# Performance work log

Hardware: AMD Instinct MI355X
Metric: run time of the kernel (lower is better)

The kernel has to match this reference:

```python
import jax, jax.numpy as jnp
import numpy as np

# Scene / model dims (match init_kwargs)
H, W, T = 128, 128, 8
N = 1024  # number of 3D (x,y,t) Gaussians, layer 0

CHOL_BOUND_3D = jnp.array([0.5, 0.0, 0.5, 0.5, 0.0, 0.5], dtype=jnp.float32)


def setup_inputs() -> dict:
    key = jax.random.key(0)
    k1, k2, k3 = jax.random.split(key, 3)
    xyz = jax.random.normal(k1, (N, 3), dtype=jnp.float32)          # raw (pre-tanh) positions
    cholesky = jax.random.uniform(k2, (N, 6), dtype=jnp.float32)    # raw cholesky params
    cholesky = cholesky.at[:, 5].add(float(T))                      # _init_layer0: data[:,5] += T
    features = jax.random.uniform(k3, (N, 3), dtype=jnp.float32)    # rgb features
    opacity = jnp.ones((N, 1), dtype=jnp.float32)                   # layer-0 opacity buffer (ones)
    background = jnp.ones((3,), dtype=jnp.float32)                  # unused by the sum-rasterizer
    return {"xyz": xyz, "cholesky": cholesky, "features": features,
            "opacity": opacity, "background": background}


def _render(xyz, cholesky, features, opacity):
    # --- project_gaussians_video ---
    # positions: tanh -> ndc (-1,1) -> pixel/frame coords (ndc2pix: 0.5*((v+1)*S - 1))
    sizes = jnp.array([W, H, T], dtype=jnp.float32)
    means = 0.5 * ((jnp.tanh(xyz) + 1.0) * sizes - 1.0)             # (N,3) in (x,y,t)
    c = cholesky + CHOL_BOUND_3D                                     # get_cholesky_elements
    # lower-triangular L, column-major packing: [L00,L10,L20,L11,L21,L22]
    L = jnp.zeros((N, 3, 3), dtype=c.dtype)
    L = L.at[:, 0, 0].set(c[:, 0]).at[:, 1, 0].set(c[:, 1]).at[:, 2, 0].set(c[:, 2])
    L = L.at[:, 1, 1].set(c[:, 3]).at[:, 2, 1].set(c[:, 4]).at[:, 2, 2].set(c[:, 5])
    cov = jnp.einsum('nij,nkj->nik', L, L)                           # Sigma = L L^T
    conic = jnp.linalg.inv(cov)                                      # (N,3,3), symmetric

    # --- rasterize_gaussians_sum_video (dense reference, no tile culling) ---
    # sigma(p) = 0.5 p^T Q p - p^T Q m + 0.5 m^T Q m, expressed as a [P,10] x [10,N] matmul
    qm = jnp.einsum('nij,nj->ni', conic, means)                      # (N,3)
    const = 0.5 * jnp.einsum('ni,ni->n', means, qm)                  # (N,)
    G = jnp.stack([0.5 * conic[:, 0, 0], 0.5 * conic[:, 1, 1], 0.5 * conic[:, 2, 2],
                   conic[:, 0, 1], conic[:, 0, 2], conic[:, 1, 2],
                   -qm[:, 0], -qm[:, 1], -qm[:, 2], const], axis=1)  # (N,10)

    ts = jnp.arange(T, dtype=jnp.float32)
    ys = jnp.arange(H, dtype=jnp.float32)
    xs = jnp.arange(W, dtype=jnp.float32)
    pt, py, px = jnp.meshgrid(ts, ys, xs, indexing='ij')             # (T,H,W) — t-major pixel order
    px, py, pt = px.ravel(), py.ravel(), pt.ravel()                  # (P,), P = T*H*W
    F = jnp.stack([px * px, py * py, pt * pt, px * py, px * pt, py * pt,
                   px, py, pt, jnp.ones_like(px)], axis=1)           # (P,10)

    sigma = F @ G.T                                                  # (P,N) — memory-bound hot loop
    wgt = jnp.exp(-sigma) * opacity[:, 0][None, :]                   # alpha per pixel/gaussian
    img = wgt @ features                                             # (P,3) alpha-weighted sum blend
    img = jnp.clip(img, 0.0, 1.0)
    # view(-1,T,H,W,3).permute(0,4,2,3,1) -> (1,3,H,W,T)
    return jnp.transpose(img.reshape(1, T, H, W, 3), (0, 4, 2, 3, 1))


def reference(xyz, cholesky, features, opacity, background):
    return _render(xyz, cholesky, features, opacity)
```

## Files before the change

### kernel.cpp

```cpp
#include <hip/hip_runtime.h>
#include <math.h>

#define HH 128
#define WW 128
#define TT 8
#define NG 1024
#define PP (HH * WW * TT)

__device__ __forceinline__ float fast_tanh(float x) {
    float e = __builtin_amdgcn_exp2f(x * 2.885390081777926814f);
    return 1.f - 2.f * __builtin_amdgcn_rcpf(e + 1.f);
}

__global__ __launch_bounds__(256) void gv_fused(
    const float* __restrict__ xyz,
    const float* __restrict__ chol,
    const float* __restrict__ feat,
    const float* __restrict__ opac,
    float* __restrict__ out)
{
    __shared__ __align__(16) float recs[NG * 8];
    __shared__ int sidx[NG];
    __shared__ int cnt_lds[4];

    const int tid = threadIdx.x;
    const int lane = tid & 63;
    const int wv = tid >> 6;
    const int r0 = blockIdx.x * 2;
    const float y0f = (float)(r0 & 127);
    const float tf  = (float)(r0 >> 7);
    const float kneg = -1.44269504088896340736f;

    int S_run = 0;
    for (int it = 0; it < NG / 256; ++it) {
        const int n = it * 256 + tid;
        float vy = xyz[n * 3 + 1];
        float c1 = chol[n * 6 + 1];
        float c3 = chol[n * 6 + 3] + 0.5f;
        float my = fmaf(fast_tanh(vy), 64.f, 63.5f);
        float syy = fmaf(c1, c1, c3 * c3);
        float d0 = my - y0f;
        float d1 = d0 - 1.f;
        float dmin = fminf(fabsf(d0), fabsf(d1));
        bool keep = dmin * dmin < 32.f * syy;

        unsigned long long mask = __ballot(keep);
        if (lane == 0) cnt_lds[wv] = (int)__popcll(mask);
        __syncthreads();
        int base = S_run;
        for (int w = 0; w < wv; ++w) base += cnt_lds[w];
        int tot = cnt_lds[0] + cnt_lds[1] + cnt_lds[2] + cnt_lds[3];
        if (keep) {
            int pos = __builtin_amdgcn_mbcnt_hi(
                          (unsigned)(mask >> 32),
                          __builtin_amdgcn_mbcnt_lo((unsigned)mask, 0));
            sidx[base + pos] = n;
        }
        S_run += tot;
        __syncthreads();
    }
    const int S = S_run;

    for (int j = tid; j < S; j += 256) {
        const int n = sidx[j];
        float vx = xyz[n * 3 + 0], vy = xyz[n * 3 + 1], vt = xyz[n * 3 + 2];
        float mx = 0.5f * ((fast_tanh(vx) + 1.f) * (float)WW - 1.f);
        float my = 0.5f * ((fast_tanh(vy) + 1.f) * (float)HH - 1.f);
        float mt = 0.5f * ((fast_tanh(vt) + 1.f) * (float)TT - 1.f);

        float c0 = chol[n * 6 + 0] + 0.5f;
        float c1 = chol[n * 6 + 1];
        float c2 = chol[n * 6 + 2] + 0.5f;
        float c3 = chol[n * 6 + 3] + 0.5f;
        float c4 = chol[n * 6 + 4];
        float c5 = chol[n * 6 + 5] + 0.5f;

        float a  = c0 * c0;
        float b  = c0 * c1;
        float cc = c0 * c2;
        float d  = c1 * c1 + c3 * c3;
        float e  = c1 * c2 + c3 * c4;
        float f  = c2 * c2 + c4 * c4 + c5 * c5;

        float A00 = d * f - e * e;
        float A01 = cc * e - b * f;
        float A02 = b * e - cc * d;
        float A11 = a * f - cc * cc;
        float A12 = b * cc - a * e;
        float A22 = a * d - b * b;
        float det = a * A00 + b * A01 + cc * A02;
        float rdet = 1.f / det;
        float Q00 = A00 * rdet, Q01 = A01 * rdet, Q02 = A02 * rdet;
        float Q11 = A11 * rdet, Q12 = A12 * rdet, Q22 = A22 * rdet;

        float qmx = Q00 * mx + Q01 * my + Q02 * mt;
        float qmy = Q01 * mx + Q11 * my + Q12 * mt;
        float qmt = Q02 * mx + Q12 * my + Q22 * mt;
        float cst = 0.5f * (mx * qmx + my * qmy + mt * qmt);

        float G0 = 0.5f * Q00, G1 = 0.5f * Q11, G2 = 0.5f * Q22;
        float G3 = Q01, G4 = Q02, G5 = Q12;
        float G6 = -qmx, G7 = -qmy, G8 = -qmt, G9 = cst;

        float u  = fmaf(G4, tf, G6);
        float v  = fmaf(G5, tf, G7);
        float w0 = fmaf(fmaf(G2, tf, G8), tf, G9);
        float B0 = fmaf(G3, y0f, u);
        float C0 = fmaf(fmaf(G1, y0f, v), y0f, w0);
        float y1f = y0f + 1.f;
        float B1 = fmaf(G3, y1f, u);
        float C1 = fmaf(fmaf(G1, y1f, v), y1f, w0);

        float op = opac[n];
        float4* l4 = (float4*)recs;
        l4[j * 2 + 0] = (float4){kneg * G0, op * feat[n * 3 + 0],
                                 op * feat[n * 3 + 1], op * feat[n * 3 + 2]};
        l4[j * 2 + 1] = (float4){kneg * B0, kneg * C0, kneg * B1, kneg * C1};
    }
    __syncthreads();

    const int rowi = wv >> 1;
    const int x = (wv & 1) * 64 + lane;
    const float xf = (float)x;
    float a0 = 0.f, a1 = 0.f, a2 = 0.f;
    const float4* lds4 = (const float4*)recs;

#pragma unroll 4
    for (int m = 0; m < S; ++m) {
        float4 af = lds4[m * 2];
        float2 bc = *(const float2*)&recs[m * 8 + 4 + 2 * rowi];
        float s = fmaf(fmaf(af.x, xf, bc.x), xf, bc.y);
        float w = __builtin_amdgcn_exp2f(s);
        a0 = fmaf(w, af.y, a0);
        a1 = fmaf(w, af.z, a1);
        a2 = fmaf(w, af.w, a2);
    }

    a0 = fminf(fmaxf(a0, 0.f), 1.f);
    a1 = fminf(fmaxf(a1, 0.f), 1.f);
    a2 = fminf(fmaxf(a2, 0.f), 1.f);

    const int r = r0 + rowi;
    const int y = r & 127, t = r >> 7;
    const int base_o = (y * WW + x) * TT + t;
    out[base_o] = a0;
    out[base_o + PP] = a1;
    out[base_o + 2 * PP] = a2;
}

extern "C" void kernel_launch(void* const* d_in, const int* in_sizes, int n_in,
                              void* d_out, int out_size, void* d_ws, size_t ws_size,
                              hipStream_t stream) {
    const float* xyz  = (const float*)d_in[0];
    const float* chol = (const float*)d_in[1];
    const float* feat = (const float*)d_in[2];
    const float* opac = (const float*)d_in[3];
    float* out = (float*)d_out;

    const int blocks = (TT * HH) / 2;
    gv_fused<<<blocks, 256, 0, stream>>>(xyz, chol, feat, opac, out);
}
```

Before: 14.36 us.

## Split fused kernel into prep pass and main raster pass using workspace

Adds a prep kernel that culls Gaussians per row-pair once, shared across all time frames, and computes each Gaussian's conic and color record once into a workspace buffer. The main kernel then reads the precomputed list and records instead of redoing culling and matrix inversion in each of the 512 blocks. This removes repeated per-block setup work but adds a second launch and global-memory round trips. The original fused kernel remains as a fallback when the workspace is too small. The prep kernel uses tanhf instead of the fast approximation.

```diff
diff --git a/kernel.cpp b/kernel.cpp
--- a/kernel.cpp
+++ b/kernel.cpp
@@ -6,10 +6,181 @@
 #define TT 8
 #define NG 1024
 #define PP (HH * WW * TT)
+#define YP 64
+
+#define REC_OFF    0
+#define SLIST_OFF  (NG * 16)
+#define SCOUNT_OFF (SLIST_OFF + YP * NG)
+#define WS_FLOATS  (SCOUNT_OFF + YP)
 
 __device__ __forceinline__ float fast_tanh(float x) {
     float e = __builtin_amdgcn_exp2f(x * 2.885390081777926814f);
     return 1.f - 2.f * __builtin_amdgcn_rcpf(e + 1.f);
+}
+
+__global__ __launch_bounds__(256) void gv_prep(
+    const float* __restrict__ xyz,
+    const float* __restrict__ chol,
+    const float* __restrict__ feat,
+    const float* __restrict__ opac,
+    float* __restrict__ ws)
+{
+    const int bid = blockIdx.x;
+    const int tid = threadIdx.x;
+
+    if (bid < YP) {
+        __shared__ int cnt_lds[4];
+        int* slist = (int*)(ws + SLIST_OFF) + bid * NG;
+        int* scount = (int*)(ws + SCOUNT_OFF);
+        const int lane = tid & 63;
+        const int wv = tid >> 6;
+        const float y0f = (float)(2 * bid);
+
+        int S_run = 0;
+        for (int it = 0; it < NG / 256; ++it) {
+            const int n = it * 256 + tid;
+            float vy = xyz[n * 3 + 1];
+            float c1 = chol[n * 6 + 1];
+            float c3 = chol[n * 6 + 3] + 0.5f;
+            float my = fmaf(tanhf(vy), 64.f, 63.5f);
+            float syy = fmaf(c1, c1, c3 * c3);
+            float d0 = my - y0f;
+            float d1 = d0 - 1.f;
+            float dmin = fminf(fabsf(d0), fabsf(d1));
+            bool keep = dmin * dmin < 32.f * syy;
+
+            unsigned long long mask = __ballot(keep);
+            if (lane == 0) cnt_lds[wv] = (int)__popcll(mask);
+            __syncthreads();
+            int base = S_run;
+            for (int w = 0; w < wv; ++w) base += cnt_lds[w];
+            int tot = cnt_lds[0] + cnt_lds[1] + cnt_lds[2] + cnt_lds[3];
+            if (keep) {
+                int pos = __builtin_amdgcn_mbcnt_hi(
+                              (unsigned)(mask >> 32),
+                              __builtin_amdgcn_mbcnt_lo((unsigned)mask, 0));
+                slist[base + pos] = n;
+            }
+            S_run += tot;
+            __syncthreads();
+        }
+        if (tid == 0) scount[bid] = S_run;
+    } else {
+        const int n = (bid - YP) * 128 + tid;
+        if (tid >= 128) return;
+
+        float vx = xyz[n * 3 + 0], vy = xyz[n * 3 + 1], vt = xyz[n * 3 + 2];
+        float mx = 0.5f * ((tanhf(vx) + 1.f) * (float)WW - 1.f);
+        float my = 0.5f * ((tanhf(vy) + 1.f) * (float)HH - 1.f);
+        float mt = 0.5f * ((tanhf(vt) + 1.f) * (float)TT - 1.f);
+
+        float c0 = chol[n * 6 + 0] + 0.5f;
+        float c1 = chol[n * 6 + 1];
+        float c2 = chol[n * 6 + 2] + 0.5f;
+        float c3 = chol[n * 6 + 3] + 0.5f;
+        float c4 = chol[n * 6 + 4];
+        float c5 = chol[n * 6 + 5] + 0.5f;
+
+        float a  = c0 * c0;
+        float b  = c0 * c1;
+        float cc = c0 * c2;
+        float d  = c1 * c1 + c3 * c3;
+        float e  = c1 * c2 + c3 * c4;
+        float f  = c2 * c2 + c4 * c4 + c5 * c5;
+
+        float A00 = d * f - e * e;
+        float A01 = cc * e - b * f;
+        float A02 = b * e - cc * d;
+        float A11 = a * f - cc * cc;
+        float A12 = b * cc - a * e;
+        float A22 = a * d - b * b;
+        float det = a * A00 + b * A01 + cc * A02;
+        float rdet = 1.f / det;
+        float Q00 = A00 * rdet, Q01 = A01 * rdet, Q02 = A02 * rdet;
+        float Q11 = A11 * rdet, Q12 = A12 * rdet, Q22 = A22 * rdet;
+
+        float qmx = Q00 * mx + Q01 * my + Q02 * mt;
+        float qmy = Q01 * mx + Q11 * my + Q12 * mt;
+        float qmt = Q02 * mx + Q12 * my + Q22 * mt;
+        float cst = 0.5f * (mx * qmx + my * qmy + mt * qmt);
+
+        float op = opac[n];
+        float4* r4 = (float4*)(ws + REC_OFF);
+        r4[n * 4 + 0] = (float4){0.5f * Q00, 0.5f * Q11, 0.5f * Q22, Q01};
+        r4[n * 4 + 1] = (float4){Q02, Q12, -qmx, -qmy};
+        r4[n * 4 + 2] = (float4){-qmt, cst, 0.f, 0.f};
+        r4[n * 4 + 3] = (float4){op * feat[n * 3 + 0], op * feat[n * 3 + 1],
+                                 op * feat[n * 3 + 2], 0.f};
+    }
+}
+
+__global__ __launch_bounds__(256) void gv_main(
+    const float* __restrict__ ws,
+    float* __restrict__ out)
+{
+    __shared__ __align__(16) float recs[NG * 8];
+
+    const int tid = threadIdx.x;
+    const int lane = tid & 63;
+    const int wv = tid >> 6;
+    const int yp = blockIdx.x & 63;
+    const int t  = blockIdx.x >> 6;
+    const float y0f = (float)(2 * yp);
+    const float tf  = (float)t;
+    const float kneg = -1.44269504088896340736f;
+
+    const int* slist = (const int*)(ws + SLIST_OFF) + yp * NG;
+    const int S = ((const int*)(ws + SCOUNT_OFF))[yp];
+    const float4* g4 = (const float4*)(ws + REC_OFF);
+
+    for (int j = tid; j < S; j += 256) {
+        const int n = slist[j];
+        float4 ra = g4[n * 4 + 0];
+        float4 rb = g4[n * 4 + 1];
+        float4 rc = g4[n * 4 + 2];
+        float4 rd = g4[n * 4 + 3];
+
+        float u  = fmaf(rb.x, tf, rb.z);
+        float v  = fmaf(rb.y, tf, rb.w);
+        float w0 = fmaf(fmaf(ra.z, tf, rc.x), tf, rc.y);
+        float B0 = fmaf(ra.w, y0f, u);
+        float C0 = fmaf(fmaf(ra.y, y0f, v), y0f, w0);
+        float y1f = y0f + 1.f;
+        float B1 = fmaf(ra.w, y1f, u);
+        float C1 = fmaf(fmaf(ra.y, y1f, v), y1f, w0);
+
+        float4* l4 = (float4*)recs;
+        l4[j * 2 + 0] = (float4){kneg * ra.x, rd.x, rd.y, rd.z};
+        l4[j * 2 + 1] = (float4){kneg * B0, kneg * C0, kneg * B1, kneg * C1};
+    }
+    __syncthreads();
+
+    const int rowi = wv >> 1;
+    const int x = (wv & 1) * 64 + lane;
+    const float xf = (float)x;
+    float a0 = 0.f, a1 = 0.f, a2 = 0.f;
+    const float4* lds4 = (const float4*)recs;
+
+#pragma unroll 4
+    for (int m = 0; m < S; ++m) {
+        float4 af = lds4[m * 2];
+        float2 bc = *(const float2*)&recs[m * 8 + 4 + 2 * rowi];
+        float s = fmaf(fmaf(af.x, xf, bc.x), xf, bc.y);
+        float w = __builtin_amdgcn_exp2f(s);
+        a0 = fmaf(w, af.y, a0);
+        a1 = fmaf(w, af.z, a1);
+        a2 = fmaf(w, af.w, a2);
+    }
+
+    a0 = fminf(fmaxf(a0, 0.f), 1.f);
+    a1 = fminf(fmaxf(a1, 0.f), 1.f);
+    a2 = fminf(fmaxf(a2, 0.f), 1.f);
+
+    const int y = 2 * yp + rowi;
+    const int base_o = (y * WW + x) * TT + t;
+    out[base_o] = a0;
+    out[base_o + PP] = a1;
+    out[base_o + 2 * PP] = a2;
 }
 
 __global__ __launch_bounds__(256) void gv_fused(
@@ -67,37 +238,26 @@
         float mx = 0.5f * ((fast_tanh(vx) + 1.f) * (float)WW - 1.f);
         float my = 0.5f * ((fast_tanh(vy) + 1.f) * (float)HH - 1.f);
         float mt = 0.5f * ((fast_tanh(vt) + 1.f) * (float)TT - 1.f);
-
         float c0 = chol[n * 6 + 0] + 0.5f;
         float c1 = chol[n * 6 + 1];
         float c2 = chol[n * 6 + 2] + 0.5f;
         float c3 = chol[n * 6 + 3] + 0.5f;
         float c4 = chol[n * 6 + 4];
         float c5 = chol[n * 6 + 5] + 0.5f;
-
-        float a  = c0 * c0;
-        float b  = c0 * c1;
-        float cc = c0 * c2;
+        float a  = c0 * c0, b = c0 * c1, cc = c0 * c2;
         float d  = c1 * c1 + c3 * c3;
         float e  = c1 * c2 + c3 * c4;
         float f  = c2 * c2 + c4 * c4 + c5 * c5;
-
-        float A00 = d * f - e * e;
-        float A01 = cc * e - b * f;
-        float A02 = b * e - cc * d;
-        float A11 = a * f - cc * cc;
-        float A12 = b * cc - a * e;
-        float A22 = a * d - b * b;
+        float A00 = d * f - e * e, A01 = cc * e - b * f, A02 = b * e - cc * d;
+        float A11 = a * f - cc * cc, A12 = b * cc - a * e, A22 = a * d - b * b;
         float det = a * A00 + b * A01 + cc * A02;
         float rdet = 1.f / det;
         float Q00 = A00 * rdet, Q01 = A01 * rdet, Q02 = A02 * rdet;
         float Q11 = A11 * rdet, Q12 = A12 * rdet, Q22 = A22 * rdet;
-
         float qmx = Q00 * mx + Q01 * my + Q02 * mt;
         float qmy = Q01 * mx + Q11 * my + Q12 * mt;
         float qmt = Q02 * mx + Q12 * my + Q22 * mt;
         float cst = 0.5f * (mx * qmx + my * qmy + mt * qmt);
-
         float G0 = 0.5f * Q00, G1 = 0.5f * Q11, G2 = 0.5f * Q22;
         float G3 = Q01, G4 = Q02, G5 = Q12;
         float G6 = -qmx, G7 = -qmy, G8 = -qmt, G9 = cst;
@@ -156,7 +316,12 @@
     const float* feat = (const float*)d_in[2];
     const float* opac = (const float*)d_in[3];
     float* out = (float*)d_out;
-
-    const int blocks = (TT * HH) / 2;
-    gv_fused<<<blocks, 256, 0, stream>>>(xyz, chol, feat, opac, out);
-}
+    float* ws  = (float*)d_ws;
+
+    if (ws_size >= (size_t)WS_FLOATS * sizeof(float)) {
+        gv_prep<<<YP + NG / 128, 256, 0, stream>>>(xyz, chol, feat, opac, ws);
+        gv_main<<<YP * TT, 256, 0, stream>>>(ws, out);
+    } else {
+        gv_fused<<<(TT * HH) / 2, 256, 0, stream>>>(xyz, chol, feat, opac, out);
+    }
+}
```

Result: slower. 17.63 us (+22.7%).

## Split Gaussian list across eight wave groups with LDS partial-sum reduction

Applied to the files above, without the earlier changes.

Each block grows from 256 to 1024 threads. The 1024 Gaussians are split into 8 slices of 128, and each pair of waves culls and preprocesses its own slice without the serial prefix-scan loop and its repeated barriers. Each wave now covers two pixels per lane (x and x+64) and accumulates over only its slice. Partial sums are then reduced through LDS by the first group. This shortens the per-thread serial loop over Gaussians and the culling serialization, at the cost of a larger block, more LDS use, an extra reduction pass and possible load imbalance between slices.

```diff
diff --git a/kernel.cpp b/kernel.cpp
--- a/kernel.cpp
+++ b/kernel.cpp
@@ -6,34 +6,38 @@
 #define TT 8
 #define NG 1024
 #define PP (HH * WW * TT)
+#define NS 8
+#define GS 128
 
 __device__ __forceinline__ float fast_tanh(float x) {
     float e = __builtin_amdgcn_exp2f(x * 2.885390081777926814f);
     return 1.f - 2.f * __builtin_amdgcn_rcpf(e + 1.f);
 }
 
-__global__ __launch_bounds__(256) void gv_fused(
+__global__ __launch_bounds__(1024, 8) void gv_fused(
     const float* __restrict__ xyz,
     const float* __restrict__ chol,
     const float* __restrict__ feat,
     const float* __restrict__ opac,
     float* __restrict__ out)
 {
-    __shared__ __align__(16) float recs[NG * 8];
-    __shared__ int sidx[NG];
-    __shared__ int cnt_lds[4];
+    __shared__ __align__(16) float recs[NS][GS * 8];
+    __shared__ int sidx[NS][GS];
+    __shared__ int cnt_lds[16];
+    __shared__ __align__(16) float4 pbuf[7][2][WW];
 
     const int tid = threadIdx.x;
     const int lane = tid & 63;
     const int wv = tid >> 6;
+    const int s = wv >> 1;
+    const int sub = wv & 1;
     const int r0 = blockIdx.x * 2;
     const float y0f = (float)(r0 & 127);
     const float tf  = (float)(r0 >> 7);
     const float kneg = -1.44269504088896340736f;
 
-    int S_run = 0;
-    for (int it = 0; it < NG / 256; ++it) {
-        const int n = it * 256 + tid;
+    {
+        const int n = s * GS + sub * 64 + lane;
         float vy = xyz[n * 3 + 1];
         float c1 = chol[n * 6 + 1];
         float c3 = chol[n * 6 + 3] + 0.5f;
@@ -45,107 +49,137 @@
         bool keep = dmin * dmin < 32.f * syy;
 
         unsigned long long mask = __ballot(keep);
-        if (lane == 0) cnt_lds[wv] = (int)__popcll(mask);
-        __syncthreads();
-        int base = S_run;
-        for (int w = 0; w < wv; ++w) base += cnt_lds[w];
-        int tot = cnt_lds[0] + cnt_lds[1] + cnt_lds[2] + cnt_lds[3];
         if (keep) {
             int pos = __builtin_amdgcn_mbcnt_hi(
                           (unsigned)(mask >> 32),
                           __builtin_amdgcn_mbcnt_lo((unsigned)mask, 0));
-            sidx[base + pos] = n;
+            sidx[s][sub * 64 + pos] = n;
         }
-        S_run += tot;
-        __syncthreads();
-    }
-    const int S = S_run;
-
-    for (int j = tid; j < S; j += 256) {
-        const int n = sidx[j];
-        float vx = xyz[n * 3 + 0], vy = xyz[n * 3 + 1], vt = xyz[n * 3 + 2];
-        float mx = 0.5f * ((fast_tanh(vx) + 1.f) * (float)WW - 1.f);
-        float my = 0.5f * ((fast_tanh(vy) + 1.f) * (float)HH - 1.f);
-        float mt = 0.5f * ((fast_tanh(vt) + 1.f) * (float)TT - 1.f);
-
-        float c0 = chol[n * 6 + 0] + 0.5f;
-        float c1 = chol[n * 6 + 1];
-        float c2 = chol[n * 6 + 2] + 0.5f;
-        float c3 = chol[n * 6 + 3] + 0.5f;
-        float c4 = chol[n * 6 + 4];
-        float c5 = chol[n * 6 + 5] + 0.5f;
-
-        float a  = c0 * c0;
-        float b  = c0 * c1;
-        float cc = c0 * c2;
-        float d  = c1 * c1 + c3 * c3;
-        float e  = c1 * c2 + c3 * c4;
-        float f  = c2 * c2 + c4 * c4 + c5 * c5;
-
-        float A00 = d * f - e * e;
-        float A01 = cc * e - b * f;
-        float A02 = b * e - cc * d;
-        float A11 = a * f - cc * cc;
-        float A12 = b * cc - a * e;
-        float A22 = a * d - b * b;
-        float det = a * A00 + b * A01 + cc * A02;
-        float rdet = 1.f / det;
-        float Q00 = A00 * rdet, Q01 = A01 * rdet, Q02 = A02 * rdet;
-        float Q11 = A11 * rdet, Q12 = A12 * rdet, Q22 = A22 * rdet;
-
-        float qmx = Q00 * mx + Q01 * my + Q02 * mt;
-        float qmy = Q01 * mx + Q11 * my + Q12 * mt;
-        float qmt = Q02 * mx + Q12 * my + Q22 * mt;
-        float cst = 0.5f * (mx * qmx + my * qmy + mt * qmt);
-
-        float G0 = 0.5f * Q00, G1 = 0.5f * Q11, G2 = 0.5f * Q22;
-        float G3 = Q01, G4 = Q02, G5 = Q12;
-        float G6 = -qmx, G7 = -qmy, G8 = -qmt, G9 = cst;
-
-        float u  = fmaf(G4, tf, G6);
-        float v  = fmaf(G5, tf, G7);
-        float w0 = fmaf(fmaf(G2, tf, G8), tf, G9);
-        float B0 = fmaf(G3, y0f, u);
-        float C0 = fmaf(fmaf(G1, y0f, v), y0f, w0);
-        float y1f = y0f + 1.f;
-        float B1 = fmaf(G3, y1f, u);
-        float C1 = fmaf(fmaf(G1, y1f, v), y1f, w0);
-
-        float op = opac[n];
-        float4* l4 = (float4*)recs;
-        l4[j * 2 + 0] = (float4){kneg * G0, op * feat[n * 3 + 0],
-                                 op * feat[n * 3 + 1], op * feat[n * 3 + 2]};
-        l4[j * 2 + 1] = (float4){kneg * B0, kneg * C0, kneg * B1, kneg * C1};
+        if (lane == 0) cnt_lds[wv] = (int)__popcll(mask);
     }
     __syncthreads();
 
-    const int rowi = wv >> 1;
-    const int x = (wv & 1) * 64 + lane;
-    const float xf = (float)x;
+    {
+        const int sb = tid >> 7;
+        const int tq = tid & 127;
+        const int cA = cnt_lds[2 * sb];
+        const int Sb = cA + cnt_lds[2 * sb + 1];
+        if (tq < Sb) {
+            const int n = (tq < cA) ? sidx[sb][tq] : sidx[sb][64 + tq - cA];
+
+            float vx = xyz[n * 3 + 0], vy = xyz[n * 3 + 1], vt = xyz[n * 3 + 2];
+            float mx = 0.5f * ((fast_tanh(vx) + 1.f) * (float)WW - 1.f);
+            float my = 0.5f * ((fast_tanh(vy) + 1.f) * (float)HH - 1.f);
+            float mt = 0.5f * ((fast_tanh(vt) + 1.f) * (float)TT - 1.f);
+
+            float c0 = chol[n * 6 + 0] + 0.5f;
+            float c1 = chol[n * 6 + 1];
+            float c2 = chol[n * 6 + 2] + 0.5f;
+            float c3 = chol[n * 6 + 3] + 0.5f;
+            float c4 = chol[n * 6 + 4];
+            float c5 = chol[n * 6 + 5] + 0.5f;
+
+            float a  = c0 * c0;
+            float b  = c0 * c1;
+            float cc = c0 * c2;
+            float d  = c1 * c1 + c3 * c3;
+            float e  = c1 * c2 + c3 * c4;
+            float f  = c2 * c2 + c4 * c4 + c5 * c5;
+
+            float A00 = d * f - e * e;
+            float A01 = cc * e - b * f;
+            float A02 = b * e - cc * d;
+            float A11 = a * f - cc * cc;
+            float A12 = b * cc - a * e;
+            float A22 = a * d - b * b;
+            float det = a * A00 + b * A01 + cc * A02;
+            float rdet = 1.f / det;
+            float Q00 = A00 * rdet, Q01 = A01 * rdet, Q02 = A02 * rdet;
+            float Q11 = A11 * rdet, Q12 = A12 * rdet, Q22 = A22 * rdet;
+
+            float qmx = Q00 * mx + Q01 * my + Q02 * mt;
+            float qmy = Q01 * mx + Q11 * my + Q12 * mt;
+            float qmt = Q02 * mx + Q12 * my + Q22 * mt;
+            float cst = 0.5f * (mx * qmx + my * qmy + mt * qmt);
+
+            float G0 = 0.5f * Q00, G1 = 0.5f * Q11, G2 = 0.5f * Q22;
+            float G3 = Q01, G4 = Q02, G5 = Q12;
+            float G6 = -qmx, G7 = -qmy, G8 = -qmt, G9 = cst;
+
+            float u  = fmaf(G4, tf, G6);
+            float v  = fmaf(G5, tf, G7);
+            float w0 = fmaf(fmaf(G2, tf, G8), tf, G9);
+            float B0 = fmaf(G3, y0f, u);
+            float C0 = fmaf(fmaf(G1, y0f, v), y0f, w0);
+            float y1f = y0f + 1.f;
+            float B1 = fmaf(G3, y1f, u);
+            float C1 = fmaf(fmaf(G1, y1f, v), y1f, w0);
+
+            float op = opac[n];
+            float4* l4 = (float4*)recs[sb];
+            l4[tq * 2 + 0] = (float4){kneg * G0, op * feat[n * 3 + 0],
+                                      op * feat[n * 3 + 1], op * feat[n * 3 + 2]};
+            l4[tq * 2 + 1] = (float4){kneg * B0, kneg * C0, kneg * B1, kneg * C1};
+        }
+    }
+    __syncthreads();
+
+    const int S = cnt_lds[2 * s] + cnt_lds[2 * s + 1];
+    const float x1 = (float)lane;
+    const float x2 = x1 + 64.f;
     float a0 = 0.f, a1 = 0.f, a2 = 0.f;
-    const float4* lds4 = (const float4*)recs;
+    float b0 = 0.f, b1 = 0.f, b2 = 0.f;
+    const float4* lds4 = (const float4*)recs[s];
+    const float* recf = recs[s];
 
 #pragma unroll 4
     for (int m = 0; m < S; ++m) {
         float4 af = lds4[m * 2];
-        float2 bc = *(const float2*)&recs[m * 8 + 4 + 2 * rowi];
-        float s = fmaf(fmaf(af.x, xf, bc.x), xf, bc.y);
-        float w = __builtin_amdgcn_exp2f(s);
-        a0 = fmaf(w, af.y, a0);
-        a1 = fmaf(w, af.z, a1);
-        a2 = fmaf(w, af.w, a2);
+        float2 bc = *(const float2*)&recf[m * 8 + 4 + 2 * sub];
+        float s1 = fmaf(fmaf(af.x, x1, bc.x), x1, bc.y);
+        float s2 = fmaf(fmaf(af.x, x2, bc.x), x2, bc.y);
+        float w1 = __builtin_amdgcn_exp2f(s1);
+        float w2 = __builtin_amdgcn_exp2f(s2);
+        a0 = fmaf(w1, af.y, a0);
+        a1 = fmaf(w1, af.z, a1);
+        a2 = fmaf(w1, af.w, a2);
+        b0 = fmaf(w2, af.y, b0);
+        b1 = fmaf(w2, af.z, b1);
+        b2 = fmaf(w2, af.w, b2);
     }
 
-    a0 = fminf(fmaxf(a0, 0.f), 1.f);
-    a1 = fminf(fmaxf(a1, 0.f), 1.f);
-    a2 = fminf(fmaxf(a2, 0.f), 1.f);
+    if (s != 0) {
+        pbuf[s - 1][sub][lane]      = (float4){a0, a1, a2, 0.f};
+        pbuf[s - 1][sub][lane + 64] = (float4){b0, b1, b2, 0.f};
+    }
+    __syncthreads();
 
-    const int r = r0 + rowi;
-    const int y = r & 127, t = r >> 7;
-    const int base_o = (y * WW + x) * TT + t;
-    out[base_o] = a0;
-    out[base_o + PP] = a1;
-    out[base_o + 2 * PP] = a2;
+    if (s == 0) {
+#pragma unroll
+        for (int k = 0; k < 7; ++k) {
+            float4 p = pbuf[k][sub][lane];
+            float4 q = pbuf[k][sub][lane + 64];
+            a0 += p.x; a1 += p.y; a2 += p.z;
+            b0 += q.x; b1 += q.y; b2 += q.z;
+        }
+
+        a0 = fminf(fmaxf(a0, 0.f), 1.f);
+        a1 = fminf(fmaxf(a1, 0.f), 1.f);
+        a2 = fminf(fmaxf(a2, 0.f), 1.f);
+        b0 = fminf(fmaxf(b0, 0.f), 1.f);
+        b1 = fminf(fmaxf(b1, 0.f), 1.f);
+        b2 = fminf(fmaxf(b2, 0.f), 1.f);
+
+        const int r = r0 + sub;
+        const int y = r & 127, t = r >> 7;
+        const int base_o = (y * WW + lane) * TT + t;
+        out[base_o] = a0;
+        out[base_o + 64 * TT] = b0;
+        out[base_o + PP] = a1;
+        out[base_o + PP + 64 * TT] = b1;
+        out[base_o + 2 * PP] = a2;
+        out[base_o + 2 * PP + 64 * TT] = b2;
+    }
 }
 
 extern "C" void kernel_launch(void* const* d_in, const int* in_sizes, int n_in,
@@ -158,5 +192,5 @@
     float* out = (float*)d_out;
 
     const int blocks = (TT * HH) / 2;
-    gv_fused<<<blocks, 256, 0, stream>>>(xyz, chol, feat, opac, out);
+    gv_fused<<<blocks, 1024, 0, stream>>>(xyz, chol, feat, opac, out);
 }
```

New measurement: 14.10 us. No clear change (-1.8%).
